# Kernel optimization log

Measured on AMD Instinct MI355X. Metric: run time of the kernel, lower is better.

Reference implementation:

```python
import jax, jax.numpy as jnp
import numpy as np

B, I, T, H = 64, 128, 1024, 256


def setup_inputs() -> dict:
    key = jax.random.key(0)
    k1, k2, k3, k4, k5 = jax.random.split(key, 5)
    s = 1.0 / np.sqrt(H)  # PyTorch LSTM init scale, keeps gates well-conditioned
    return {
        "x": jax.random.normal(k1, (B, I, T), dtype=jnp.float32),
        "W_ih": jax.random.normal(k2, (4 * H, I), dtype=jnp.float32) * s,
        "W_hh": jax.random.normal(k3, (4 * H, H), dtype=jnp.float32) * s,
        "b_ih": jax.random.normal(k4, (4 * H,), dtype=jnp.float32) * s,
        "b_hh": jax.random.normal(k5, (4 * H,), dtype=jnp.float32) * s,
    }


def reference(x, W_ih, W_hh, b_ih, b_hh):
    # x: [B, I, T] -> permute to [B, T, I] (batch_first LSTM input)
    xt = jnp.transpose(x, (0, 2, 1))
    bsz, tlen, _ = xt.shape
    hid = W_hh.shape[1]
    # Precompute input contribution to all gates: [B, T, 4H]
    pre = jnp.einsum("bti,gi->btg", xt, W_ih) + b_ih + b_hh

    def step(carry, p_t):
        h, c = carry  # [B, H] each
        gates = p_t + h @ W_hh.T  # [B, 4H]
        i, f, g, o = jnp.split(gates, 4, axis=-1)  # PyTorch gate order i,f,g,o
        i = jax.nn.sigmoid(i)
        f = jax.nn.sigmoid(f)
        g = jnp.tanh(g)
        o = jax.nn.sigmoid(o)
        c = f * c + i * g
        h = o * jnp.tanh(c)
        return (h, c), h

    h0 = jnp.zeros((bsz, hid), dtype=x.dtype)
    c0 = jnp.zeros((bsz, hid), dtype=x.dtype)
    _, hs = jax.lax.scan(step, (h0, c0), jnp.transpose(pre, (1, 0, 2)))  # hs: [T, B, H]
    # ReLU then permute back to [B, H, T]
    return jax.nn.relu(jnp.transpose(hs, (1, 2, 0)))
```

## Files before the change

### kernel.cpp

```cpp
#include <hip/hip_runtime.h>
#include <cstdint>
#include <cstddef>

typedef _Float16 f16;
typedef _Float16 f16x2 __attribute__((ext_vector_type(2)));

constexpr int Bn = 64, In = 128, Tn = 1024, Hn = 256, Gn = 1024;
constexpr int WREG = 192;
constexpr int NCH  = 16;


__device__ __forceinline__ float fdot2(f16x2 a, f16x2 b, float c) {
#if defined(__has_builtin)
#if __has_builtin(__builtin_amdgcn_fdot2)
  return __builtin_amdgcn_fdot2(a, b, c, false);
#else
  return c + (float)a.x * (float)b.x + (float)a.y * (float)b.y;
#endif
#else
  return c + (float)a.x * (float)b.x + (float)a.y * (float)b.y;
#endif
}

__device__ __forceinline__ float rcp_(float x) {
#if defined(__has_builtin)
#if __has_builtin(__builtin_amdgcn_rcpf)
  return __builtin_amdgcn_rcpf(x);
#else
  return 1.f / x;
#endif
#else
  return 1.f / x;
#endif
}

__device__ __forceinline__ float sigm(float x) {
  return rcp_(1.f + __expf(-x));
}

__device__ __forceinline__ float tanh_(float x) {
  float xc = fminf(fmaxf(x, -15.f), 15.f);
  float e = __expf(-2.f * xc);
  return (1.f - e) * rcp_(1.f + e);
}

union F4H { float4 f4; f16x2 h2[4]; };

__global__ void pack_whh(const float* __restrict__ Whh,
                         f16x2* __restrict__ wreg, f16x2* __restrict__ wlds) {
  const int j = blockIdx.x;
  const int k = threadIdx.x;
  int row, col2;
  if (k < 128)       { row = j;       col2 = k; }
  else if (k < WREG) { row = j + 512; col2 = k - 128; }
  else               { row = j + 512; col2 = 64 + (k - WREG); }
  const float2* w2 = (const float2*)Whh;
  float2 v = w2[(size_t)row * (Hn / 2) + col2];
  f16x2 h; h.x = (f16)v.x; h.y = (f16)v.y;
  if (k < WREG) {
    wreg[(size_t)k * 512 + j] = h;
  } else {
    int idx = k - WREG;
    int q = idx >> 2, m = idx & 3;
    wlds[((size_t)q * 512 + j) * 4 + m] = h;
  }
}

__global__ __launch_bounds__(256, 4) void gemm_pre(
    const float* __restrict__ x, const float* __restrict__ Wih,
    const float* __restrict__ bih, const float* __restrict__ bhh,
    float* __restrict__ pre, int Ts, int tbase) {
  __shared__ float xs[64][64];
  __shared__ float wsh[64][65];
  const int bb = blockIdx.z, t0 = blockIdx.y * 64, g0 = blockIdx.x * 64;
  const int tid = threadIdx.x;
  const int tx = tid & 15, ty = tid >> 4;
  const int l64 = tid & 63, h2b = tid >> 6;
  float acc[4][4] = {};

  for (int ih = 0; ih < 2; ++ih) {
#pragma unroll 4
    for (int s = 0; s < 16; ++s) {
      int i = h2b + s * 4;
      xs[i][l64] = x[(size_t)bb * In * Tn + (size_t)(ih * 64 + i) * Tn + tbase + t0 + l64];
      wsh[i][l64] = Wih[(size_t)(g0 + i) * In + ih * 64 + l64];
    }
    __syncthreads();
#pragma unroll 8
    for (int i = 0; i < 64; ++i) {
      float4 xv = *(const float4*)&xs[i][ty * 4];
      float w0 = wsh[tx * 4 + 0][i];
      float w1 = wsh[tx * 4 + 1][i];
      float w2 = wsh[tx * 4 + 2][i];
      float w3 = wsh[tx * 4 + 3][i];
      acc[0][0] += xv.x * w0; acc[0][1] += xv.x * w1; acc[0][2] += xv.x * w2; acc[0][3] += xv.x * w3;
      acc[1][0] += xv.y * w0; acc[1][1] += xv.y * w1; acc[1][2] += xv.y * w2; acc[1][3] += xv.y * w3;
      acc[2][0] += xv.z * w0; acc[2][1] += xv.z * w1; acc[2][2] += xv.z * w2; acc[2][3] += xv.z * w3;
      acc[3][0] += xv.w * w0; acc[3][1] += xv.w * w1; acc[3][2] += xv.w * w2; acc[3][3] += xv.w * w3;
    }
    __syncthreads();
  }

  float bs[4];
#pragma unroll
  for (int q = 0; q < 4; ++q) {
    int g = g0 + tx * 4 + q;
    bs[q] = bih[g] + bhh[g];
  }
#pragma unroll
  for (int ti = 0; ti < 4; ++ti) {
    int tl = t0 + ty * 4 + ti;
    size_t idx = ((size_t)bb * Ts + tl) * Gn + g0 + tx * 4;
    float4 fv;
    fv.x = acc[ti][0] + bs[0]; fv.y = acc[ti][1] + bs[1];
    fv.z = acc[ti][2] + bs[2]; fv.w = acc[ti][3] + bs[3];
    *(float4*)&pre[idx] = fv;
  }
}

__global__ __launch_bounds__(512, 2) void lstm_rec(
    const f16x2* __restrict__ wreg, const float4* __restrict__ wldsg,
    const float* __restrict__ pre, float* __restrict__ out,
    float* __restrict__ cws, f16x2* __restrict__ hws,
    int seg0, int Ts, int tbase) {
  __shared__ float4 wlds4[NCH * 512];
  __shared__ f16x2  hbuf[128];
  __shared__ float  ig[256];
  __shared__ f16    hist[256 * 33];

  const int j  = threadIdx.x;
  const int bb = blockIdx.x;

  f16x2 w[WREG];
#pragma unroll
  for (int k = 0; k < WREG; ++k) w[k] = wreg[(size_t)k * 512 + j];
#pragma unroll
  for (int q = 0; q < NCH; ++q) wlds4[q * 512 + j] = wldsg[(size_t)q * 512 + j];
  if (j < 128) {
    f16x2 z = {};
    hbuf[j] = seg0 ? z : hws[bb * 128 + j];
  }
  __syncthreads();

  const size_t pbase = (size_t)bb * Ts * Gn;
  float* outb = out + (size_t)bb * Hn * Tn + tbase;

  float c = 0.f;
  if (j >= 256 && !seg0) c = cws[bb * 256 + (j - 256)];
  float p0 = pre[pbase + j];
  float p1 = pre[pbase + 512 + j];

  const float4* hv4 = (const float4*)hbuf;

  for (int t = 0; t < Ts; ++t) {
    float a0 = 0.f, a1 = 0.f, b0 = 0.f, b1 = 0.f;
#pragma unroll
    for (int k0 = 0; k0 < 16; ++k0) {
      F4H hu; hu.f4 = hv4[k0];
      a0 = fdot2(w[4 * k0 + 0], hu.h2[0], a0);
      a1 = fdot2(w[4 * k0 + 1], hu.h2[1], a1);
      a0 = fdot2(w[4 * k0 + 2], hu.h2[2], a0);
      a1 = fdot2(w[4 * k0 + 3], hu.h2[3], a1);
      b0 = fdot2(w[128 + 4 * k0 + 0], hu.h2[0], b0);
      b1 = fdot2(w[128 + 4 * k0 + 1], hu.h2[1], b1);
      b0 = fdot2(w[128 + 4 * k0 + 2], hu.h2[2], b0);
      b1 = fdot2(w[128 + 4 * k0 + 3], hu.h2[3], b1);
    }
#pragma unroll
    for (int k0 = 16; k0 < 32; ++k0) {
      F4H hu; hu.f4 = hv4[k0];
      F4H wu; wu.f4 = wlds4[(k0 - 16) * 512 + j];
      a0 = fdot2(w[4 * k0 + 0], hu.h2[0], a0);
      a1 = fdot2(w[4 * k0 + 1], hu.h2[1], a1);
      a0 = fdot2(w[4 * k0 + 2], hu.h2[2], a0);
      a1 = fdot2(w[4 * k0 + 3], hu.h2[3], a1);
      b0 = fdot2(wu.h2[0], hu.h2[0], b0);
      b1 = fdot2(wu.h2[1], hu.h2[1], b1);
      b0 = fdot2(wu.h2[2], hu.h2[2], b0);
      b1 = fdot2(wu.h2[3], hu.h2[3], b1);
    }
    float g0raw = a0 + a1 + p0;
    float g1raw = b0 + b1 + p1;

    if (t + 1 < Ts) {
      size_t o = pbase + (size_t)(t + 1) * Gn + j;
      p0 = pre[o];
      p1 = pre[o + 512];
    }

    float act0, act1;
    if (j < 256) {
      act0 = sigm(g0raw);
      act1 = tanh_(g1raw);
      ig[j] = act0 * act1;
    } else {
      act0 = sigm(g0raw);
      act1 = sigm(g1raw);
    }
    __syncthreads();
    if (j >= 256) {
      int n = j - 256;
      c = act0 * c + ig[n];
      float th = tanh_(c);
      float h = act1 * th;
      hist[n * 33 + (t & 31)] = (f16)fmaxf(h, 0.f);
      ((f16*)hbuf)[n] = (f16)h;
    }
    __syncthreads();

    if ((t & 31) == 31) {
      int t0 = t - 31;
#pragma unroll
      for (int v = 0; v < 16; ++v) {
        int flat = v * 512 + j;
        int n = flat >> 5, tt = flat & 31;
        outb[(size_t)n * Tn + t0 + tt] = (float)hist[n * 33 + tt];
      }
    }
  }

  if (j >= 256) cws[bb * 256 + (j - 256)] = c;
  if (j < 128) hws[bb * 128 + j] = hbuf[j];
}

extern "C" void kernel_launch(void* const* d_in, const int* in_sizes, int n_in,
                              void* d_out, int out_size, void* d_ws, size_t ws_size,
                              hipStream_t stream) {
  const float* x   = (const float*)d_in[0];
  const float* Wih = (const float*)d_in[1];
  const float* Whh = (const float*)d_in[2];
  const float* bih = (const float*)d_in[3];
  const float* bhh = (const float*)d_in[4];
  float* out = (float*)d_out;
  char* ws = (char*)d_ws;

  f16x2* wreg  = (f16x2*)ws;
  f16x2* wldsg = (f16x2*)(ws + 384 * 1024);
  float* cws   = (float*)(ws + 512 * 1024);
  f16x2* hws   = (f16x2*)(ws + 576 * 1024);
  float* pre   = (float*)(ws + (1 << 20));

  int Ts = 64;
  for (int cand = 1024; cand >= 64; cand >>= 1) {
    size_t need = (size_t)(1 << 20) + (size_t)Bn * cand * Gn * 4;
    if (need <= ws_size) { Ts = cand; break; }
  }
  int nseg = Tn / Ts;

  pack_whh<<<dim3(512), dim3(256), 0, stream>>>(Whh, wreg, wldsg);

  for (int s = 0; s < nseg; ++s) {
    dim3 gg(16, Ts / 64, 64);
    gemm_pre<<<gg, dim3(256), 0, stream>>>(x, Wih, bih, bhh, pre, Ts, s * Ts);
    lstm_rec<<<dim3(64), dim3(512), 0, stream>>>(
        wreg, (const float4*)wldsg, pre, out, cws, hws, (s == 0) ? 1 : 0, Ts, s * Ts);
  }
}
```

Measured before the change: 15.24 ms.

## Use one thread per gate row in LSTM recurrence with 1024-thread blocks

The recurrent kernel now launches 1024 threads per batch block, so each thread computes a single gate row instead of two. Each thread keeps 96 f16x2 weight pairs in registers and streams the other 32 pairs from LDS. Gate activations go through a shared gact array before the 256 cell-update threads combine them. This halves the serial dot-product chain per thread on the latency-bound time loop, at the cost of more threads per barrier and register pressure under a 1024-thread launch bound.

```diff
diff --git a/kernel.cpp b/kernel.cpp
--- a/kernel.cpp
+++ b/kernel.cpp
@@ -6,8 +6,6 @@
 typedef _Float16 f16x2 __attribute__((ext_vector_type(2)));
 
 constexpr int Bn = 64, In = 128, Tn = 1024, Hn = 256, Gn = 1024;
-constexpr int WREG = 192;
-constexpr int NCH  = 16;
 
 
 __device__ __forceinline__ float fdot2(f16x2 a, f16x2 b, float c) {
@@ -44,25 +42,21 @@
   return (1.f - e) * rcp_(1.f + e);
 }
 
-union F4H { float4 f4; f16x2 h2[4]; };
+#define BC2(x) __builtin_bit_cast(f16x2, x)
 
 __global__ void pack_whh(const float* __restrict__ Whh,
-                         f16x2* __restrict__ wreg, f16x2* __restrict__ wlds) {
-  const int j = blockIdx.x;
+                         f16x2* __restrict__ wregG, f16x2* __restrict__ wldsE) {
+  const int n = blockIdx.x;
   const int k = threadIdx.x;
-  int row, col2;
-  if (k < 128)       { row = j;       col2 = k; }
-  else if (k < WREG) { row = j + 512; col2 = k - 128; }
-  else               { row = j + 512; col2 = 64 + (k - WREG); }
   const float2* w2 = (const float2*)Whh;
-  float2 v = w2[(size_t)row * (Hn / 2) + col2];
+  float2 v = w2[(size_t)n * (Hn / 2) + k];
   f16x2 h; h.x = (f16)v.x; h.y = (f16)v.y;
-  if (k < WREG) {
-    wreg[(size_t)k * 512 + j] = h;
+  if (k < 96) {
+    wregG[(size_t)k * 1024 + n] = h;
   } else {
-    int idx = k - WREG;
+    int idx = k - 96;
     int q = idx >> 2, m = idx & 3;
-    wlds[((size_t)q * 512 + j) * 4 + m] = h;
+    wldsE[((size_t)(q << 10) + n) * 4 + m] = h;
   }
 }
 
@@ -118,27 +112,50 @@
   }
 }
 
-__global__ __launch_bounds__(512, 2) void lstm_rec(
-    const f16x2* __restrict__ wreg, const float4* __restrict__ wldsg,
+#define LDW(i) const f16x2 w##i = wregG[(size_t)(i) * 1024 + n];
+#define DOT4(K0, K1, K2, K3, CC)            \
+  {                                         \
+    float4 hv = hv4[CC];                    \
+    a0 = fdot2(w##K0, BC2(hv.x), a0);       \
+    a1 = fdot2(w##K1, BC2(hv.y), a1);       \
+    a0 = fdot2(w##K2, BC2(hv.z), a0);       \
+    a1 = fdot2(w##K3, BC2(hv.w), a1);       \
+  }
+
+__global__ __launch_bounds__(1024, 1)
+void lstm_rec(
+    const f16x2* __restrict__ wregG, const float4* __restrict__ wldsG,
     const float* __restrict__ pre, float* __restrict__ out,
     float* __restrict__ cws, f16x2* __restrict__ hws,
     int seg0, int Ts, int tbase) {
-  __shared__ float4 wlds4[NCH * 512];
-  __shared__ f16x2  hbuf[128];
-  __shared__ float  ig[256];
-  __shared__ f16    hist[256 * 33];
-
-  const int j  = threadIdx.x;
+  __shared__ float4 wl4[8 * 1024];
+  __shared__ __align__(16) f16 hbuf[256];
+  __shared__ float gact[1024];
+  __shared__ f16 hist[256 * 33];
+
+  const int n  = threadIdx.x;
   const int bb = blockIdx.x;
 
-  f16x2 w[WREG];
-#pragma unroll
-  for (int k = 0; k < WREG; ++k) w[k] = wreg[(size_t)k * 512 + j];
-#pragma unroll
-  for (int q = 0; q < NCH; ++q) wlds4[q * 512 + j] = wldsg[(size_t)q * 512 + j];
-  if (j < 128) {
+  LDW(0)  LDW(1)  LDW(2)  LDW(3)  LDW(4)  LDW(5)  LDW(6)  LDW(7)
+  LDW(8)  LDW(9)  LDW(10) LDW(11) LDW(12) LDW(13) LDW(14) LDW(15)
+  LDW(16) LDW(17) LDW(18) LDW(19) LDW(20) LDW(21) LDW(22) LDW(23)
+  LDW(24) LDW(25) LDW(26) LDW(27) LDW(28) LDW(29) LDW(30) LDW(31)
+  LDW(32) LDW(33) LDW(34) LDW(35) LDW(36) LDW(37) LDW(38) LDW(39)
+  LDW(40) LDW(41) LDW(42) LDW(43) LDW(44) LDW(45) LDW(46) LDW(47)
+  LDW(48) LDW(49) LDW(50) LDW(51) LDW(52) LDW(53) LDW(54) LDW(55)
+  LDW(56) LDW(57) LDW(58) LDW(59) LDW(60) LDW(61) LDW(62) LDW(63)
+  LDW(64) LDW(65) LDW(66) LDW(67) LDW(68) LDW(69) LDW(70) LDW(71)
+  LDW(72) LDW(73) LDW(74) LDW(75) LDW(76) LDW(77) LDW(78) LDW(79)
+  LDW(80) LDW(81) LDW(82) LDW(83) LDW(84) LDW(85) LDW(86) LDW(87)
+  LDW(88) LDW(89) LDW(90) LDW(91) LDW(92) LDW(93) LDW(94) LDW(95)
+
+#pragma unroll
+  for (int q = 0; q < 8; ++q) wl4[(q << 10) + n] = wldsG[(size_t)(q << 10) + n];
+
+  f16x2* hbuf2 = (f16x2*)hbuf;
+  if (n < 128) {
     f16x2 z = {};
-    hbuf[j] = seg0 ? z : hws[bb * 128 + j];
+    hbuf2[n] = seg0 ? z : hws[bb * 128 + n];
   }
   __syncthreads();
 
@@ -146,81 +163,58 @@
   float* outb = out + (size_t)bb * Hn * Tn + tbase;
 
   float c = 0.f;
-  if (j >= 256 && !seg0) c = cws[bb * 256 + (j - 256)];
-  float p0 = pre[pbase + j];
-  float p1 = pre[pbase + 512 + j];
+  if (n < 256 && !seg0) c = cws[bb * 256 + n];
+  float p = pre[pbase + n];
 
   const float4* hv4 = (const float4*)hbuf;
 
   for (int t = 0; t < Ts; ++t) {
-    float a0 = 0.f, a1 = 0.f, b0 = 0.f, b1 = 0.f;
-#pragma unroll
-    for (int k0 = 0; k0 < 16; ++k0) {
-      F4H hu; hu.f4 = hv4[k0];
-      a0 = fdot2(w[4 * k0 + 0], hu.h2[0], a0);
-      a1 = fdot2(w[4 * k0 + 1], hu.h2[1], a1);
-      a0 = fdot2(w[4 * k0 + 2], hu.h2[2], a0);
-      a1 = fdot2(w[4 * k0 + 3], hu.h2[3], a1);
-      b0 = fdot2(w[128 + 4 * k0 + 0], hu.h2[0], b0);
-      b1 = fdot2(w[128 + 4 * k0 + 1], hu.h2[1], b1);
-      b0 = fdot2(w[128 + 4 * k0 + 2], hu.h2[2], b0);
-      b1 = fdot2(w[128 + 4 * k0 + 3], hu.h2[3], b1);
-    }
-#pragma unroll
-    for (int k0 = 16; k0 < 32; ++k0) {
-      F4H hu; hu.f4 = hv4[k0];
-      F4H wu; wu.f4 = wlds4[(k0 - 16) * 512 + j];
-      a0 = fdot2(w[4 * k0 + 0], hu.h2[0], a0);
-      a1 = fdot2(w[4 * k0 + 1], hu.h2[1], a1);
-      a0 = fdot2(w[4 * k0 + 2], hu.h2[2], a0);
-      a1 = fdot2(w[4 * k0 + 3], hu.h2[3], a1);
-      b0 = fdot2(wu.h2[0], hu.h2[0], b0);
-      b1 = fdot2(wu.h2[1], hu.h2[1], b1);
-      b0 = fdot2(wu.h2[2], hu.h2[2], b0);
-      b1 = fdot2(wu.h2[3], hu.h2[3], b1);
-    }
-    float g0raw = a0 + a1 + p0;
-    float g1raw = b0 + b1 + p1;
-
-    if (t + 1 < Ts) {
-      size_t o = pbase + (size_t)(t + 1) * Gn + j;
-      p0 = pre[o];
-      p1 = pre[o + 512];
-    }
-
-    float act0, act1;
-    if (j < 256) {
-      act0 = sigm(g0raw);
-      act1 = tanh_(g1raw);
-      ig[j] = act0 * act1;
-    } else {
-      act0 = sigm(g0raw);
-      act1 = sigm(g1raw);
-    }
-    __syncthreads();
-    if (j >= 256) {
-      int n = j - 256;
-      c = act0 * c + ig[n];
+    float a0 = 0.f, a1 = 0.f;
+    DOT4(0, 1, 2, 3, 0)     DOT4(4, 5, 6, 7, 1)     DOT4(8, 9, 10, 11, 2)   DOT4(12, 13, 14, 15, 3)
+    DOT4(16, 17, 18, 19, 4) DOT4(20, 21, 22, 23, 5) DOT4(24, 25, 26, 27, 6) DOT4(28, 29, 30, 31, 7)
+    DOT4(32, 33, 34, 35, 8) DOT4(36, 37, 38, 39, 9) DOT4(40, 41, 42, 43, 10) DOT4(44, 45, 46, 47, 11)
+    DOT4(48, 49, 50, 51, 12) DOT4(52, 53, 54, 55, 13) DOT4(56, 57, 58, 59, 14) DOT4(60, 61, 62, 63, 15)
+    DOT4(64, 65, 66, 67, 16) DOT4(68, 69, 70, 71, 17) DOT4(72, 73, 74, 75, 18) DOT4(76, 77, 78, 79, 19)
+    DOT4(80, 81, 82, 83, 20) DOT4(84, 85, 86, 87, 21) DOT4(88, 89, 90, 91, 22) DOT4(92, 93, 94, 95, 23)
+#pragma unroll
+    for (int q = 0; q < 8; ++q) {
+      float4 wv = wl4[(q << 10) + n];
+      float4 hv = hv4[24 + q];
+      a0 = fdot2(BC2(wv.x), BC2(hv.x), a0);
+      a1 = fdot2(BC2(wv.y), BC2(hv.y), a1);
+      a0 = fdot2(BC2(wv.z), BC2(hv.z), a0);
+      a1 = fdot2(BC2(wv.w), BC2(hv.w), a1);
+    }
+    float raw = a0 + a1 + p;
+
+    if (t + 1 < Ts) p = pre[pbase + (size_t)(t + 1) * Gn + n];
+
+    float act = (n >= 512 && n < 768) ? tanh_(raw) : sigm(raw);
+    gact[n] = act;
+    __syncthreads();
+
+    if (n < 256) {
+      c = gact[256 + n] * c + gact[n] * gact[512 + n];
       float th = tanh_(c);
-      float h = act1 * th;
+      float h = gact[768 + n] * th;
       hist[n * 33 + (t & 31)] = (f16)fmaxf(h, 0.f);
-      ((f16*)hbuf)[n] = (f16)h;
+      hbuf[n] = (f16)h;
     }
     __syncthreads();
 
     if ((t & 31) == 31) {
       int t0 = t - 31;
 #pragma unroll
-      for (int v = 0; v < 16; ++v) {
-        int flat = v * 512 + j;
-        int n = flat >> 5, tt = flat & 31;
-        outb[(size_t)n * Tn + t0 + tt] = (float)hist[n * 33 + tt];
+      for (int v = 0; v < 8; ++v) {
+        int flat = (v << 10) + n;
+        int row = flat >> 5, tt = flat & 31;
+        outb[(size_t)row * Tn + t0 + tt] = (float)hist[row * 33 + tt];
       }
     }
   }
 
-  if (j >= 256) cws[bb * 256 + (j - 256)] = c;
-  if (j < 128) hws[bb * 128 + j] = hbuf[j];
+  if (n < 256) cws[bb * 256 + n] = c;
+  if (n < 128) hws[bb * 128 + n] = hbuf2[n];
 }
 
 extern "C" void kernel_launch(void* const* d_in, const int* in_sizes, int n_in,
@@ -234,8 +228,8 @@
   float* out = (float*)d_out;
   char* ws = (char*)d_ws;
 
-  f16x2* wreg  = (f16x2*)ws;
-  f16x2* wldsg = (f16x2*)(ws + 384 * 1024);
+  f16x2* wregG = (f16x2*)ws;
+  f16x2* wldsE = (f16x2*)(ws + 384 * 1024);
   float* cws   = (float*)(ws + 512 * 1024);
   f16x2* hws   = (f16x2*)(ws + 576 * 1024);
   float* pre   = (float*)(ws + (1 << 20));
@@ -247,12 +241,12 @@
   }
   int nseg = Tn / Ts;
 
-  pack_whh<<<dim3(512), dim3(256), 0, stream>>>(Whh, wreg, wldsg);
+  pack_whh<<<dim3(1024), dim3(128), 0, stream>>>(Whh, wregG, wldsE);
 
   for (int s = 0; s < nseg; ++s) {
     dim3 gg(16, Ts / 64, 64);
     gemm_pre<<<gg, dim3(256), 0, stream>>>(x, Wih, bih, bhh, pre, Ts, s * Ts);
-    lstm_rec<<<dim3(64), dim3(512), 0, stream>>>(
-        wreg, (const float4*)wldsg, pre, out, cws, hws, (s == 0) ? 1 : 0, Ts, s * Ts);
-  }
-}
+    lstm_rec<<<dim3(64), dim3(1024), 0, stream>>>(
+        wregG, (const float4*)wldsE, pre, out, cws, hws, (s == 0) ? 1 : 0, Ts, s * Ts);
+  }
+}
```

New measurement: 37.06 ms. 143% more time.
